# Kernel tuning notes

Measured on AMD Instinct MI355X. Metric: run time of the kernel, lower is better.

## Reference

```python
import jax, jax.numpy as jnp
import numpy as np

B, N1, N2, E = 8, 32, 32, 256
H = 8                 # num_heads == args.vir_heads
KD = E // H           # key dim per head = 32
HD = E // H           # head dim (value_dim == embed_dim)
L = N1 * N2           # 1024 tokens
SCALING = KD ** -0.5
LN_EPS = 1e-5


def _rel_pos_2d():
    # RetNetRelPosDeform2D with zero offsets (vir_use_deformable=False)
    half = 1.0 / 10000.0 ** jnp.linspace(0.0, 1.0, KD // 2)
    angle = jnp.repeat(half, 2)                                   # (KD,) interleaved pairs
    decay = jnp.log(1.0 - 2.0 ** (-2.0 - 5.0 * jnp.arange(H, dtype=jnp.float32) / H))  # (H,)
    i1 = jnp.arange(N1, dtype=jnp.float32)
    i2 = jnp.arange(N2, dtype=jnp.float32)
    index_k = (i1[:, None] + i2[None, :]).reshape(L)              # (L,)
    sin_k = jnp.sin(index_k[:, None] * angle[None, :])            # (L, KD)
    cos_k = jnp.cos(index_k[:, None] * angle[None, :])
    # zero offsets => index_q == index_k, broadcast over (B, H)
    sin_q = sin_k[None, None]                                     # (1,1,L,KD)
    cos_q = cos_k[None, None]
    # Manhattan distance decay mask on the 2D grid
    d = (jnp.abs(i1[:, None, None, None] - i1[None, None, :, None])
         + jnp.abs(i2[None, :, None, None] - i2[None, None, None, :])).reshape(L, L)
    mask = jnp.exp(d[None, :, :] * decay[:, None, None])          # (H, L, L)
    mask = jnp.nan_to_num(mask)
    mask = mask / jnp.sqrt(mask.sum(-1, keepdims=True))
    return sin_q, cos_q, sin_k, cos_k, mask


def rotate_every_two(x):
    x1 = x[..., ::2]
    x2 = x[..., 1::2]
    return jnp.stack((-x2, x1), axis=-1).reshape(x.shape)


def theta_shift(x, sin, cos):
    return x * cos + rotate_every_two(x) * sin


def setup_inputs() -> dict:
    key = jax.random.key(0)
    ks = jax.random.split(key, 5)
    gain_qkv = 2.0 ** -2.5 * (6.0 / (E + E)) ** 0.5  # xavier_uniform bound scale
    gain_o = 2.0 ** -1 * (6.0 / (E + E)) ** 0.5
    x = jax.random.normal(ks[0], (B, N1, N2, E), dtype=jnp.float32)
    Wq = jax.random.uniform(ks[1], (E, E), jnp.float32, -gain_qkv, gain_qkv)
    Wk = jax.random.uniform(ks[2], (E, E), jnp.float32, -gain_qkv, gain_qkv)
    Wv = jax.random.uniform(ks[3], (E, E), jnp.float32, -gain_qkv, gain_qkv)
    Wo = jax.random.uniform(ks[4], (E, E), jnp.float32, -gain_o, gain_o)
    ln_g = jnp.ones((HD,), jnp.float32)
    ln_b = jnp.zeros((HD,), jnp.float32)
    return {"x": x, "Wq": Wq, "Wk": Wk, "Wv": Wv, "Wo": Wo, "ln_g": ln_g, "ln_b": ln_b}


def reference(x, Wq, Wk, Wv, Wo, ln_g, ln_b):
    sin_q, cos_q, sin_k, cos_k, mask = _rel_pos_2d()
    xf = x.reshape(B, L, E)
    q = (xf @ Wq.T).reshape(B, L, H, KD).transpose(0, 2, 1, 3)    # (B,H,L,KD)
    k = (xf @ Wk.T * SCALING).reshape(B, L, H, KD).transpose(0, 2, 1, 3)
    vr = (xf @ Wv.T).reshape(B, L, H, HD).transpose(0, 2, 1, 3)   # (B,H,L,HD)
    qr = theta_shift(q, sin_q, cos_q)
    kr = theta_shift(k, sin_k[None, None], cos_k[None, None])
    qk = jnp.einsum('bhqd,bhkd->bhqk', qr, kr) * mask[None]       # (B,H,L,L)
    den = jnp.clip(jax.lax.stop_gradient(jnp.abs(qk)).sum(-1, keepdims=True), 1.0, 5e4)
    qk = qk / den
    out = jnp.einsum('bhqk,bhkd->bhqd', qk, vr).transpose(0, 2, 1, 3)  # (B,L,H,HD)
    mu = out.mean(-1, keepdims=True)
    var = out.var(-1, keepdims=True)
    out = (out - mu) / jnp.sqrt(var + LN_EPS) * ln_g + ln_b       # per-head LayerNorm
    out = jax.nn.gelu(out.reshape(B, L, H * HD), approximate=False)
    out = out @ Wo.T
    return out.reshape(B, N1, N2, E)
```

## Files before the change

### kernel.cpp

```cpp
#include <hip/hip_runtime.h>
#include <math.h>

typedef unsigned short u16;
typedef unsigned int u32;
typedef unsigned long long u64;
typedef __bf16 bf16x8 __attribute__((ext_vector_type(8)));
typedef short s16x4 __attribute__((ext_vector_type(4)));
typedef float f32x4 __attribute__((ext_vector_type(4)));

#define SCALING 0.17677669529663687f
#define LOG2E 1.44269504088896f
#define LOG2_10000 13.287712379549449f

__device__ __forceinline__ u16 f2bf(float f) {
    u32 u; __builtin_memcpy(&u, &f, 4);
    u = u + 0x7FFFu + ((u >> 16) & 1u);
    return (u16)(u >> 16);
}
__device__ __forceinline__ u32 fbits(float f) {
    u32 u; __builtin_memcpy(&u, &f, 4); return u;
}
__device__ __forceinline__ u32 pack_bf16(float lo, float hi) {
    return __builtin_amdgcn_perm(fbits(hi) + 0x8000u, fbits(lo) + 0x8000u, 0x07060302u);
}
__device__ __forceinline__ f32x4 mfma16(bf16x8 a, bf16x8 b, f32x4 c) {
    return __builtin_amdgcn_mfma_f32_16x16x32_bf16(a, b, c, 0, 0, 0);
}
__device__ __forceinline__ f32x4 mfma_k16(u64 a, u64 b, f32x4 c) {
#if __has_builtin(__builtin_amdgcn_mfma_f32_16x16x16bf16_1k)
    s16x4 av, bv;
    __builtin_memcpy(&av, &a, 8); __builtin_memcpy(&bv, &b, 8);
    return __builtin_amdgcn_mfma_f32_16x16x16bf16_1k(av, bv, c, 0, 0, 0);
#elif __has_builtin(__builtin_amdgcn_mfma_f32_16x16x16_bf16)
    typedef __bf16 bf16x4_t __attribute__((ext_vector_type(4)));
    bf16x4_t av, bv;
    __builtin_memcpy(&av, &a, 8); __builtin_memcpy(&bv, &b, 8);
    return __builtin_amdgcn_mfma_f32_16x16x16_bf16(av, bv, c, 0, 0, 0);
#else
    f32x4 d = c;
    asm volatile("v_mfma_f32_16x16x16_bf16 %0, %1, %2, %0\n\ts_nop 4"
                 : "+v"(d) : "v"(a), "v"(b));
    return d;
#endif
}
__device__ __forceinline__ float decay_l2(int h) {
    return logf(1.0f - exp2f(-2.0f - 0.625f * (float)h)) * LOG2E;
}

__global__ __launch_bounds__(256) void tc_kernel(float2* __restrict__ tc) {
    int idx = blockIdx.x * 256 + threadIdx.x;
    int l = idx >> 5, d = idx & 31;
    float ang = exp2f(-LOG2_10000 * (1.0f / 15.0f) * (float)(d >> 1));
    float idl = (float)((l >> 5) + (l & 31));
    float sv, cv;
    __sincosf(idl * ang, &sv, &cv);
    tc[idx] = make_float2(cv, (d & 1) ? sv : -sv);
}

template<int AF32>
__global__ __launch_bounds__(256) void gemm_bt_kernel(
    const void* __restrict__ Av,
    const float* __restrict__ W0, const float* __restrict__ W1, const float* __restrict__ W2,
    const float2* __restrict__ tc,
    u16* __restrict__ O0, u16* __restrict__ O1, u16* __restrict__ O2,
    float* __restrict__ Of, int mode_base) {
    __shared__ __align__(16) u16 As[64 * 136];
    __shared__ __align__(16) u16 Ws[64 * 136];
    int z = blockIdx.z;
    const float* W = (z == 0) ? W0 : (z == 1) ? W1 : W2;
    u16* O = (z == 0) ? O0 : (z == 1) ? O1 : O2;
    int mode = mode_base + z;
    int n0 = blockIdx.x * 64, r0 = blockIdx.y * 64;
    int tid = threadIdx.x;
    int w = tid >> 6, lane = tid & 63, ln = lane & 15, quad = lane >> 4;
    f32x4 acc[4] = {};
#pragma unroll
    for (int ch = 0; ch < 2; ch++) {
        int k0 = ch * 128;
        if (ch) __syncthreads();
#pragma unroll
        for (int i = 0; i < 8; i++) {
            int c = tid + i * 256;
            int row = c >> 5, seg = c & 31;
            float4 wv = *(const float4*)&W[(long)(n0 + row) * 256 + k0 + seg * 4];
            union { int2 v; u16 s[4]; } t;
            t.s[0] = f2bf(wv.x); t.s[1] = f2bf(wv.y); t.s[2] = f2bf(wv.z); t.s[3] = f2bf(wv.w);
            *(int2*)&Ws[row * 136 + seg * 4] = t.v;
        }
        if (AF32) {
            const float* A = (const float*)Av;
#pragma unroll
            for (int i = 0; i < 8; i++) {
                int c = tid + i * 256;
                int row = c >> 5, seg = c & 31;
                float4 av = *(const float4*)&A[(long)(r0 + row) * 256 + k0 + seg * 4];
                union { int2 v; u16 s[4]; } t;
                t.s[0] = f2bf(av.x); t.s[1] = f2bf(av.y); t.s[2] = f2bf(av.z); t.s[3] = f2bf(av.w);
                *(int2*)&As[row * 136 + seg * 4] = t.v;
            }
        } else {
            const u16* A = (const u16*)Av;
#pragma unroll
            for (int i = 0; i < 4; i++) {
                int c = tid + i * 256;
                int row = c >> 4, seg = c & 15;
                *(int4*)&As[row * 136 + seg * 8] = *(const int4*)&A[(long)(r0 + row) * 256 + k0 + seg * 8];
            }
        }
        __syncthreads();
#pragma unroll
        for (int kt = 0; kt < 4; kt++) {
            bf16x8 a = *(const bf16x8*)&As[(w * 16 + ln) * 136 + kt * 32 + quad * 8];
#pragma unroll
            for (int nt = 0; nt < 4; nt++) {
                bf16x8 b = *(const bf16x8*)&Ws[(nt * 16 + ln) * 136 + kt * 32 + quad * 8];
                acc[nt] = mfma16(a, b, acc[nt]);
            }
        }
    }
    int rowg = r0 + w * 16 + quad * 4;
    if (mode == 3) {
#pragma unroll
        for (int nt = 0; nt < 4; nt++) {
            int e = n0 + nt * 16 + ln;
#pragma unroll
            for (int r = 0; r < 4; r++)
                Of[(long)(rowg + r) * 256 + e] = acc[nt][r];
        }
        return;
    }
    float scl = (mode == 1) ? SCALING : 1.0f;
#pragma unroll
    for (int nt = 0; nt < 4; nt++) {
        int e = n0 + nt * 16 + ln;
        int d = e & 31, hh = e >> 5;
#pragma unroll
        for (int r = 0; r < 4; r++) {
            int gi = rowg + r;
            int b = gi >> 10, l = gi & 1023;
            float v = acc[nt][r] * scl;
            float p = __shfl_xor(v, 1);
            float res;
            if (mode == 2) {
                res = v;
            } else {
                float2 sc = tc[l * 32 + d];
                res = v * sc.x + p * sc.y;
            }
            O[(((long)(b * 8 + hh)) * 1024 + l) * 32 + d] = f2bf(res);
        }
    }
}

__global__ __launch_bounds__(256) void attn_kernel(
    const u16* __restrict__ qr, const u16* __restrict__ kr, const u16* __restrict__ vr,
    const float* __restrict__ lng, const float* __restrict__ lnb,
    u16* __restrict__ out) {
    __shared__ __align__(16) u16 Qs[64 * 40];
    __shared__ __align__(16) u16 Ks[2][64 * 40];
    __shared__ __align__(16) u32 VtW[2][32 * 36];
    __shared__ float Tt[64];
    __shared__ float Ss[32];
    int b = blockIdx.z, h = blockIdx.y, q0 = blockIdx.x * 64;
    int tid = threadIdx.x, w = tid >> 6, lane = tid & 63, ln = lane & 15, quad = lane >> 4;
    long bh = b * 8 + h;
    const u16* qb = qr + bh * 32768;
    const u16* kb = kr + bh * 32768;
    const u16* vb = vr + bh * 32768;
    float dec = decay_l2(h);
    {
        int row = tid >> 2, seg = tid & 3;
        *(int4*)&Qs[row * 40 + seg * 8] = *(const int4*)&qb[(q0 + row) * 32 + seg * 8];
    }
    if (tid < 63) Tt[tid] = exp2f(dec * (float)tid);
    int krow = tid >> 2, kseg = tid & 3;
    int vp = tid >> 3, vseg = tid & 7;
    int4 kreg = *(const int4*)&kb[(long)krow * 32 + kseg * 8];
    int2 v0 = *(const int2*)&vb[(long)(vp * 2) * 32 + vseg * 4];
    int2 v1 = *(const int2*)&vb[(long)(vp * 2 + 1) * 32 + vseg * 4];
    __syncthreads();
    bf16x8 aq = *(const bf16x8*)&Qs[(w * 16 + ln) * 40 + quad * 8];
    int q = q0 + w * 16 + ln;
    int q1i = q >> 5, q2i = q & 31;
    float bt[2][4];
#pragma unroll
    for (int s2 = 0; s2 < 2; s2++)
#pragma unroll
        for (int r = 0; r < 4; r++)
            bt[s2][r] = Tt[abs(q2i - (s2 * 16 + quad * 4 + r))];
    if (tid < 32) {
        float s = 0.0f;
#pragma unroll
        for (int b2 = 0; b2 < 32; b2++) s += Tt[abs(tid - b2)];
        Ss[tid] = s;
    }
    *(int4*)&Ks[0][krow * 40 + kseg * 8] = kreg;
    VtW[0][(vseg * 4 + 0) * 36 + vp] = __builtin_amdgcn_perm(v1.x, v0.x, 0x05040100u);
    VtW[0][(vseg * 4 + 1) * 36 + vp] = __builtin_amdgcn_perm(v1.x, v0.x, 0x07060302u);
    VtW[0][(vseg * 4 + 2) * 36 + vp] = __builtin_amdgcn_perm(v1.y, v0.y, 0x05040100u);
    VtW[0][(vseg * 4 + 3) * 36 + vp] = __builtin_amdgcn_perm(v1.y, v0.y, 0x07060302u);
    kreg = *(const int4*)&kb[(long)(64 + krow) * 32 + kseg * 8];
    v0 = *(const int2*)&vb[(long)(64 + vp * 2) * 32 + vseg * 4];
    v1 = *(const int2*)&vb[(long)(64 + vp * 2 + 1) * 32 + vseg * 4];
    __syncthreads();
    float rqv = rsqrtf(Ss[q1i] * Ss[q2i]);
    f32x4 accO0 = {}, accO1 = {};
    float den = 0.0f;
    for (int kt = 0; kt < 16; kt++) {
        int cur = kt & 1;
        float a0 = Tt[abs(q1i - 2 * kt)] * rqv;
        float a1 = Tt[abs(q1i - 2 * kt - 1)] * rqv;
        const u16* ksb = &Ks[cur][0];
        const u32* vtb = &VtW[cur][0];
#pragma unroll
        for (int nt = 0; nt < 4; nt++) {
            bf16x8 ak = *(const bf16x8*)&ksb[(nt * 16 + ln) * 40 + quad * 8];
            f32x4 s = mfma16(ak, aq, (f32x4){0.f, 0.f, 0.f, 0.f});
            float aa = (nt & 2) ? a1 : a0;
            float p0 = s[0] * aa * bt[nt & 1][0];
            float p1 = s[1] * aa * bt[nt & 1][1];
            float p2 = s[2] * aa * bt[nt & 1][2];
            float p3 = s[3] * aa * bt[nt & 1][3];
            den += fabsf(p0); den += fabsf(p1); den += fabsf(p2); den += fabsf(p3);
            u32 blo = pack_bf16(p0, p1), bhi = pack_bf16(p2, p3);
            u64 bb = ((u64)bhi << 32) | blo;
            u64 av0 = *(const u64*)&vtb[ln * 36 + nt * 8 + quad * 2];
            u64 av1 = *(const u64*)&vtb[(16 + ln) * 36 + nt * 8 + quad * 2];
            accO0 = mfma_k16(av0, bb, accO0);
            accO1 = mfma_k16(av1, bb, accO1);
        }
        if (kt < 15) {
            int nb = 1 - cur;
            *(int4*)&Ks[nb][krow * 40 + kseg * 8] = kreg;
            VtW[nb][(vseg * 4 + 0) * 36 + vp] = __builtin_amdgcn_perm(v1.x, v0.x, 0x05040100u);
            VtW[nb][(vseg * 4 + 1) * 36 + vp] = __builtin_amdgcn_perm(v1.x, v0.x, 0x07060302u);
            VtW[nb][(vseg * 4 + 2) * 36 + vp] = __builtin_amdgcn_perm(v1.y, v0.y, 0x05040100u);
            VtW[nb][(vseg * 4 + 3) * 36 + vp] = __builtin_amdgcn_perm(v1.y, v0.y, 0x07060302u);
            if (kt < 14) {
                int t2 = (kt + 2) * 64;
                kreg = *(const int4*)&kb[(long)(t2 + krow) * 32 + kseg * 8];
                v0 = *(const int2*)&vb[(long)(t2 + vp * 2) * 32 + vseg * 4];
                v1 = *(const int2*)&vb[(long)(t2 + vp * 2 + 1) * 32 + vseg * 4];
            }
            __syncthreads();
        }
    }
    den += __shfl_xor(den, 16);
    den += __shfl_xor(den, 32);
    float id = 1.0f / fminf(fmaxf(den, 1.0f), 50000.0f);
    float o[8];
#pragma unroll
    for (int r = 0; r < 4; r++) { o[r] = accO0[r] * id; o[4 + r] = accO1[r] * id; }
    float s1 = 0.0f, s2 = 0.0f;
#pragma unroll
    for (int i = 0; i < 8; i++) { s1 += o[i]; s2 += o[i] * o[i]; }
    s1 += __shfl_xor(s1, 16); s1 += __shfl_xor(s1, 32);
    s2 += __shfl_xor(s2, 16); s2 += __shfl_xor(s2, 32);
    float mean = s1 * (1.0f / 32.0f);
    float var = s2 * (1.0f / 32.0f) - mean * mean;
    float rstd = rsqrtf(var + 1e-5f);
    float xg[8];
#pragma unroll
    for (int nv = 0; nv < 2; nv++)
#pragma unroll
        for (int r = 0; r < 4; r++) {
            int d = nv * 16 + quad * 4 + r;
            float xv = (o[nv * 4 + r] - mean) * rstd * lng[d] + lnb[d];
            xg[nv * 4 + r] = 0.5f * xv * (1.0f + erff(xv * 0.70710678118654752f));
        }
    u16* orow = out + ((long)(b * 1024 + q)) * 256 + h * 32;
    int2 st0, st1;
    st0.x = (int)pack_bf16(xg[0], xg[1]); st0.y = (int)pack_bf16(xg[2], xg[3]);
    st1.x = (int)pack_bf16(xg[4], xg[5]); st1.y = (int)pack_bf16(xg[6], xg[7]);
    *(int2*)&orow[quad * 4] = st0;
    *(int2*)&orow[16 + quad * 4] = st1;
}

extern "C" void kernel_launch(void* const* d_in, const int* in_sizes, int n_in,
                              void* d_out, int out_size, void* d_ws, size_t ws_size,
                              hipStream_t stream) {
    const float* x   = (const float*)d_in[0];
    const float* Wq  = (const float*)d_in[1];
    const float* Wk  = (const float*)d_in[2];
    const float* Wv  = (const float*)d_in[3];
    const float* Wo  = (const float*)d_in[4];
    const float* lng = (const float*)d_in[5];
    const float* lnb = (const float*)d_in[6];
    float* outp = (float*)d_out;

    u16* qr    = (u16*)d_ws;
    u16* kr    = qr + 2097152;
    u16* vr    = kr + 2097152;
    u16* attnb = vr + 2097152;
    float2* tc = (float2*)(attnb + 2097152);

    tc_kernel<<<128, 256, 0, stream>>>(tc);
    gemm_bt_kernel<1><<<dim3(4, 128, 3), 256, 0, stream>>>(x, Wq, Wk, Wv, tc, qr, kr, vr, nullptr, 0);
    attn_kernel<<<dim3(16, 8, 8), 256, 0, stream>>>(qr, kr, vr, lng, lnb, attnb);
    gemm_bt_kernel<0><<<dim3(4, 128, 1), 256, 0, stream>>>(attnb, Wo, Wo, Wo, tc, nullptr, nullptr, nullptr, outp, 3);
}
```

Measured before the change: 120.5 us.

## Pre-convert inputs to bf16 once, and widen attention blocks to 128 queries

After: 113.5 us. 1.06x faster.

```diff
diff --git a/kernel.cpp b/kernel.cpp
--- a/kernel.cpp
+++ b/kernel.cpp
@@ -21,7 +21,13 @@
     u32 u; __builtin_memcpy(&u, &f, 4); return u;
 }
 __device__ __forceinline__ u32 pack_bf16(float lo, float hi) {
+#if __has_builtin(__builtin_amdgcn_cvt_pk_bf16_f32)
+    typedef __bf16 bf16x2_t __attribute__((ext_vector_type(2)));
+    bf16x2_t r = __builtin_amdgcn_cvt_pk_bf16_f32(lo, hi);
+    u32 u; __builtin_memcpy(&u, &r, 4); return u;
+#else
     return __builtin_amdgcn_perm(fbits(hi) + 0x8000u, fbits(lo) + 0x8000u, 0x07060302u);
+#endif
 }
 __device__ __forceinline__ f32x4 mfma16(bf16x8 a, bf16x8 b, f32x4 c) {
     return __builtin_amdgcn_mfma_f32_16x16x32_bf16(a, b, c, 0, 0, 0);
@@ -47,27 +53,48 @@
     return logf(1.0f - exp2f(-2.0f - 0.625f * (float)h)) * LOG2E;
 }
 
-__global__ __launch_bounds__(256) void tc_kernel(float2* __restrict__ tc) {
-    int idx = blockIdx.x * 256 + threadIdx.x;
-    int l = idx >> 5, d = idx & 31;
-    float ang = exp2f(-LOG2_10000 * (1.0f / 15.0f) * (float)(d >> 1));
-    float idl = (float)((l >> 5) + (l & 31));
-    float sv, cv;
-    __sincosf(idl * ang, &sv, &cv);
-    tc[idx] = make_float2(cv, (d & 1) ? sv : -sv);
-}
-
-template<int AF32>
+__global__ __launch_bounds__(256) void prep_kernel(
+    const float* __restrict__ x,
+    const float* __restrict__ Wq, const float* __restrict__ Wk,
+    const float* __restrict__ Wv, const float* __restrict__ Wo,
+    u16* __restrict__ xb, u16* __restrict__ wb, float2* __restrict__ tc) {
+    int bid = blockIdx.x;
+    if (bid >= 1152) {
+        int idx = (bid - 1152) * 256 + threadIdx.x;
+        int l = idx >> 5, d = idx & 31;
+        float ang = exp2f(-LOG2_10000 * (1.0f / 15.0f) * (float)(d >> 1));
+        float idl = (float)((l >> 5) + (l & 31));
+        float sv, cv;
+        __sincosf(idl * ang, &sv, &cv);
+        tc[idx] = make_float2(cv, (d & 1) ? sv : -sv);
+        return;
+    }
+    const float* src; u16* dst; int off;
+    if (bid < 1024) { src = x; dst = xb; off = bid * 2048; }
+    else {
+        int wsel = (bid - 1024) >> 5;
+        src = (wsel == 0) ? Wq : (wsel == 1) ? Wk : (wsel == 2) ? Wv : Wo;
+        dst = wb + wsel * 65536;
+        off = ((bid - 1024) & 31) * 2048;
+    }
+    int i = off + threadIdx.x * 8;
+    float4 a = *(const float4*)&src[i];
+    float4 b = *(const float4*)&src[i + 4];
+    int4 t;
+    t.x = (int)pack_bf16(a.x, a.y); t.y = (int)pack_bf16(a.z, a.w);
+    t.z = (int)pack_bf16(b.x, b.y); t.w = (int)pack_bf16(b.z, b.w);
+    *(int4*)&dst[i] = t;
+}
+
 __global__ __launch_bounds__(256) void gemm_bt_kernel(
-    const void* __restrict__ Av,
-    const float* __restrict__ W0, const float* __restrict__ W1, const float* __restrict__ W2,
+    const u16* __restrict__ A, const u16* __restrict__ Wb,
     const float2* __restrict__ tc,
     u16* __restrict__ O0, u16* __restrict__ O1, u16* __restrict__ O2,
     float* __restrict__ Of, int mode_base) {
     __shared__ __align__(16) u16 As[64 * 136];
     __shared__ __align__(16) u16 Ws[64 * 136];
     int z = blockIdx.z;
-    const float* W = (z == 0) ? W0 : (z == 1) ? W1 : W2;
+    const u16* W = Wb + z * 65536;
     u16* O = (z == 0) ? O0 : (z == 1) ? O1 : O2;
     int mode = mode_base + z;
     int n0 = blockIdx.x * 64, r0 = blockIdx.y * 64;
@@ -79,33 +106,11 @@
         int k0 = ch * 128;
         if (ch) __syncthreads();
 #pragma unroll
-        for (int i = 0; i < 8; i++) {
+        for (int i = 0; i < 4; i++) {
             int c = tid + i * 256;
-            int row = c >> 5, seg = c & 31;
-            float4 wv = *(const float4*)&W[(long)(n0 + row) * 256 + k0 + seg * 4];
-            union { int2 v; u16 s[4]; } t;
-            t.s[0] = f2bf(wv.x); t.s[1] = f2bf(wv.y); t.s[2] = f2bf(wv.z); t.s[3] = f2bf(wv.w);
-            *(int2*)&Ws[row * 136 + seg * 4] = t.v;
-        }
-        if (AF32) {
-            const float* A = (const float*)Av;
-#pragma unroll
-            for (int i = 0; i < 8; i++) {
-                int c = tid + i * 256;
-                int row = c >> 5, seg = c & 31;
-                float4 av = *(const float4*)&A[(long)(r0 + row) * 256 + k0 + seg * 4];
-                union { int2 v; u16 s[4]; } t;
-                t.s[0] = f2bf(av.x); t.s[1] = f2bf(av.y); t.s[2] = f2bf(av.z); t.s[3] = f2bf(av.w);
-                *(int2*)&As[row * 136 + seg * 4] = t.v;
-            }
-        } else {
-            const u16* A = (const u16*)Av;
-#pragma unroll
-            for (int i = 0; i < 4; i++) {
-                int c = tid + i * 256;
-                int row = c >> 4, seg = c & 15;
-                *(int4*)&As[row * 136 + seg * 8] = *(const int4*)&A[(long)(r0 + row) * 256 + k0 + seg * 8];
-            }
+            int row = c >> 4, seg = c & 15;
+            *(int4*)&As[row * 136 + seg * 8] = *(const int4*)&A[(long)(r0 + row) * 256 + k0 + seg * 8];
+            *(int4*)&Ws[row * 136 + seg * 8] = *(const int4*)&W[(long)(n0 + row) * 256 + k0 + seg * 8];
         }
         __syncthreads();
 #pragma unroll
@@ -152,16 +157,16 @@
     }
 }
 
-__global__ __launch_bounds__(256) void attn_kernel(
+__global__ __launch_bounds__(512) void attn_kernel(
     const u16* __restrict__ qr, const u16* __restrict__ kr, const u16* __restrict__ vr,
     const float* __restrict__ lng, const float* __restrict__ lnb,
     u16* __restrict__ out) {
-    __shared__ __align__(16) u16 Qs[64 * 40];
+    __shared__ __align__(16) u16 Qs[128 * 40];
     __shared__ __align__(16) u16 Ks[2][64 * 40];
     __shared__ __align__(16) u32 VtW[2][32 * 36];
     __shared__ float Tt[64];
     __shared__ float Ss[32];
-    int b = blockIdx.z, h = blockIdx.y, q0 = blockIdx.x * 64;
+    int b = blockIdx.z, h = blockIdx.y, q0 = blockIdx.x * 128;
     int tid = threadIdx.x, w = tid >> 6, lane = tid & 63, ln = lane & 15, quad = lane >> 4;
     long bh = b * 8 + h;
     const u16* qb = qr + bh * 32768;
@@ -173,43 +178,51 @@
         *(int4*)&Qs[row * 40 + seg * 8] = *(const int4*)&qb[(q0 + row) * 32 + seg * 8];
     }
     if (tid < 63) Tt[tid] = exp2f(dec * (float)tid);
-    int krow = tid >> 2, kseg = tid & 3;
-    int vp = tid >> 3, vseg = tid & 7;
-    int4 kreg = *(const int4*)&kb[(long)krow * 32 + kseg * 8];
-    int2 v0 = *(const int2*)&vb[(long)(vp * 2) * 32 + vseg * 4];
-    int2 v1 = *(const int2*)&vb[(long)(vp * 2 + 1) * 32 + vseg * 4];
+    bool isK = (tid < 256);
+    int krow = (tid & 255) >> 2, kseg = tid & 3;
+    int vt = tid & 255, vp = vt >> 3, vseg = vt & 7;
+    int4 kreg; int2 v0, v1;
+    if (isK) {
+        kreg = *(const int4*)&kb[(long)krow * 32 + kseg * 8];
+    } else {
+        v0 = *(const int2*)&vb[(long)(vp * 2) * 32 + vseg * 4];
+        v1 = *(const int2*)&vb[(long)(vp * 2 + 1) * 32 + vseg * 4];
+    }
     __syncthreads();
     bf16x8 aq = *(const bf16x8*)&Qs[(w * 16 + ln) * 40 + quad * 8];
     int q = q0 + w * 16 + ln;
     int q1i = q >> 5, q2i = q & 31;
-    float bt[2][4];
-#pragma unroll
-    for (int s2 = 0; s2 < 2; s2++)
-#pragma unroll
-        for (int r = 0; r < 4; r++)
-            bt[s2][r] = Tt[abs(q2i - (s2 * 16 + quad * 4 + r))];
     if (tid < 32) {
         float s = 0.0f;
 #pragma unroll
         for (int b2 = 0; b2 < 32; b2++) s += Tt[abs(tid - b2)];
         Ss[tid] = s;
     }
-    *(int4*)&Ks[0][krow * 40 + kseg * 8] = kreg;
-    VtW[0][(vseg * 4 + 0) * 36 + vp] = __builtin_amdgcn_perm(v1.x, v0.x, 0x05040100u);
-    VtW[0][(vseg * 4 + 1) * 36 + vp] = __builtin_amdgcn_perm(v1.x, v0.x, 0x07060302u);
-    VtW[0][(vseg * 4 + 2) * 36 + vp] = __builtin_amdgcn_perm(v1.y, v0.y, 0x05040100u);
-    VtW[0][(vseg * 4 + 3) * 36 + vp] = __builtin_amdgcn_perm(v1.y, v0.y, 0x07060302u);
-    kreg = *(const int4*)&kb[(long)(64 + krow) * 32 + kseg * 8];
-    v0 = *(const int2*)&vb[(long)(64 + vp * 2) * 32 + vseg * 4];
-    v1 = *(const int2*)&vb[(long)(64 + vp * 2 + 1) * 32 + vseg * 4];
+    if (isK) {
+        *(int4*)&Ks[0][krow * 40 + kseg * 8] = kreg;
+        kreg = *(const int4*)&kb[(long)(64 + krow) * 32 + kseg * 8];
+    } else {
+        VtW[0][(vseg * 4 + 0) * 36 + vp] = __builtin_amdgcn_perm(v1.x, v0.x, 0x05040100u);
+        VtW[0][(vseg * 4 + 1) * 36 + vp] = __builtin_amdgcn_perm(v1.x, v0.x, 0x07060302u);
+        VtW[0][(vseg * 4 + 2) * 36 + vp] = __builtin_amdgcn_perm(v1.y, v0.y, 0x05040100u);
+        VtW[0][(vseg * 4 + 3) * 36 + vp] = __builtin_amdgcn_perm(v1.y, v0.y, 0x07060302u);
+        v0 = *(const int2*)&vb[(long)(64 + vp * 2) * 32 + vseg * 4];
+        v1 = *(const int2*)&vb[(long)(64 + vp * 2 + 1) * 32 + vseg * 4];
+    }
     __syncthreads();
     float rqv = rsqrtf(Ss[q1i] * Ss[q2i]);
+    float bt[2][4];
+#pragma unroll
+    for (int s2 = 0; s2 < 2; s2++)
+#pragma unroll
+        for (int r = 0; r < 4; r++)
+            bt[s2][r] = Tt[abs(q2i - (s2 * 16 + quad * 4 + r))] * rqv;
     f32x4 accO0 = {}, accO1 = {};
     float den = 0.0f;
     for (int kt = 0; kt < 16; kt++) {
         int cur = kt & 1;
-        float a0 = Tt[abs(q1i - 2 * kt)] * rqv;
-        float a1 = Tt[abs(q1i - 2 * kt - 1)] * rqv;
+        float a0 = Tt[abs(q1i - 2 * kt)];
+        float a1 = Tt[abs(q1i - 2 * kt - 1)];
         const u16* ksb = &Ks[cur][0];
         const u32* vtb = &VtW[cur][0];
 #pragma unroll
@@ -231,16 +244,20 @@
         }
         if (kt < 15) {
             int nb = 1 - cur;
-            *(int4*)&Ks[nb][krow * 40 + kseg * 8] = kreg;
-            VtW[nb][(vseg * 4 + 0) * 36 + vp] = __builtin_amdgcn_perm(v1.x, v0.x, 0x05040100u);
-            VtW[nb][(vseg * 4 + 1) * 36 + vp] = __builtin_amdgcn_perm(v1.x, v0.x, 0x07060302u);
-            VtW[nb][(vseg * 4 + 2) * 36 + vp] = __builtin_amdgcn_perm(v1.y, v0.y, 0x05040100u);
-            VtW[nb][(vseg * 4 + 3) * 36 + vp] = __builtin_amdgcn_perm(v1.y, v0.y, 0x07060302u);
-            if (kt < 14) {
-                int t2 = (kt + 2) * 64;
-                kreg = *(const int4*)&kb[(long)(t2 + krow) * 32 + kseg * 8];
-                v0 = *(const int2*)&vb[(long)(t2 + vp * 2) * 32 + vseg * 4];
-                v1 = *(const int2*)&vb[(long)(t2 + vp * 2 + 1) * 32 + vseg * 4];
+            if (isK) {
+                *(int4*)&Ks[nb][krow * 40 + kseg * 8] = kreg;
+                if (kt < 14)
+                    kreg = *(const int4*)&kb[(long)((kt + 2) * 64 + krow) * 32 + kseg * 8];
+            } else {
+                VtW[nb][(vseg * 4 + 0) * 36 + vp] = __builtin_amdgcn_perm(v1.x, v0.x, 0x05040100u);
+                VtW[nb][(vseg * 4 + 1) * 36 + vp] = __builtin_amdgcn_perm(v1.x, v0.x, 0x07060302u);
+                VtW[nb][(vseg * 4 + 2) * 36 + vp] = __builtin_amdgcn_perm(v1.y, v0.y, 0x05040100u);
+                VtW[nb][(vseg * 4 + 3) * 36 + vp] = __builtin_amdgcn_perm(v1.y, v0.y, 0x07060302u);
+                if (kt < 14) {
+                    int t2 = (kt + 2) * 64;
+                    v0 = *(const int2*)&vb[(long)(t2 + vp * 2) * 32 + vseg * 4];
+                    v1 = *(const int2*)&vb[(long)(t2 + vp * 2 + 1) * 32 + vseg * 4];
+                }
             }
             __syncthreads();
         }
@@ -288,14 +305,16 @@
     const float* lnb = (const float*)d_in[6];
     float* outp = (float*)d_out;
 
-    u16* qr    = (u16*)d_ws;
+    u16* xb    = (u16*)d_ws;
+    u16* wb    = xb + 2097152;
+    u16* qr    = wb + 262144;
     u16* kr    = qr + 2097152;
     u16* vr    = kr + 2097152;
     u16* attnb = vr + 2097152;
     float2* tc = (float2*)(attnb + 2097152);
 
-    tc_kernel<<<128, 256, 0, stream>>>(tc);
-    gemm_bt_kernel<1><<<dim3(4, 128, 3), 256, 0, stream>>>(x, Wq, Wk, Wv, tc, qr, kr, vr, nullptr, 0);
-    attn_kernel<<<dim3(16, 8, 8), 256, 0, stream>>>(qr, kr, vr, lng, lnb, attnb);
-    gemm_bt_kernel<0><<<dim3(4, 128, 1), 256, 0, stream>>>(attnb, Wo, Wo, Wo, tc, nullptr, nullptr, nullptr, outp, 3);
-}
+    prep_kernel<<<1280, 256, 0, stream>>>(x, Wq, Wk, Wv, Wo, xb, wb, tc);
+    gemm_bt_kernel<<<dim3(4, 128, 3), 256, 0, stream>>>(xb, wb, tc, qr, kr, vr, nullptr, 0);
+    attn_kernel<<<dim3(8, 8, 8), 512, 0, stream>>>(qr, kr, vr, lng, lnb, attnb);
+    gemm_bt_kernel<<<dim3(4, 128, 1), 256, 0, stream>>>(attnb, wb + 3 * 65536, tc, nullptr, nullptr, nullptr, outp, 3);
+}
```
